# Performance work log

Measured on AMD Instinct MI355X. Metric: run time of the kernel, lower is better.

The kernel has to match this reference:

```python
import jax, jax.numpy as jnp
import numpy as np

N, E, G = 50000, 1600000, 512
H, NF_IN, NF_OUT, GF_OUT, EDIM, DEPTH = 128, 64, 64, 128, 16, 3
EPS = 1e-5


def seg_softmax(logits, seg, num):
    m = jax.ops.segment_max(logits, seg, num_segments=num)
    e = jnp.exp(logits - m[seg])
    s = jax.ops.segment_sum(e, seg, num_segments=num)
    return e / s[seg]


def batchnorm_train(x, gamma, beta):
    mu = jnp.mean(x, axis=0)
    var = jnp.mean((x - mu) ** 2, axis=0)  # biased, as torch BN training
    return (x - mu) * jax.lax.rsqrt(var + EPS) * gamma + beta


def setup_inputs() -> dict:
    key = jax.random.key(0)
    ks = jax.random.split(key, 20)
    inp = {}
    inp['x'] = jax.random.normal(ks[0], (N, NF_IN), jnp.float32)
    inp['edge_index'] = jax.random.randint(ks[1], (2, E), 0, N, jnp.int64)
    inp['edge_attr'] = jax.random.normal(ks[2], (E, EDIM), jnp.float32)
    inp['batch'] = jnp.sort(jax.random.randint(ks[3], (N,), 0, G, jnp.int64))
    inp['num_graphs'] = G
    s = 0.05
    inp['Wi'] = jax.random.normal(ks[4], (H, NF_IN), jnp.float32) * s
    inp['bi'] = jnp.zeros((H,), jnp.float32)
    inp['gat_W'] = jax.random.normal(ks[5], (DEPTH, H, 2 * H), jnp.float32) * s
    inp['gat_a'] = jax.random.normal(ks[6], (DEPTH, 2 * H), jnp.float32) * s
    inp['nfW1'] = jax.random.normal(ks[7], (H, H), jnp.float32) * s
    inp['nfb1'] = jnp.zeros((H,), jnp.float32)
    inp['nf_g'] = jnp.ones((H,), jnp.float32)
    inp['nf_b'] = jnp.zeros((H,), jnp.float32)
    inp['nfW2'] = jax.random.normal(ks[8], (NF_OUT, H), jnp.float32) * s
    inp['nfb2'] = jnp.zeros((NF_OUT,), jnp.float32)
    inp['gfW1'] = jax.random.normal(ks[9], (H, H), jnp.float32) * s
    inp['gfb1'] = jnp.zeros((H,), jnp.float32)
    inp['gf_g'] = jnp.ones((H,), jnp.float32)
    inp['gf_b'] = jnp.zeros((H,), jnp.float32)
    inp['gfW2'] = jax.random.normal(ks[10], (GF_OUT, H), jnp.float32) * s
    inp['gfb2'] = jnp.zeros((GF_OUT,), jnp.float32)
    return inp


def reference(x, edge_index, edge_attr, batch, num_graphs, Wi, bi, gat_W, gat_a,
              nfW1, nfb1, nf_g, nf_b, nfW2, nfb2,
              gfW1, gfb1, gf_g, gf_b, gfW2, gfb2):
    src, dst = edge_index[0], edge_index[1]
    nf = x @ Wi.T + bi  # [N,H]
    for i in range(DEPTH):
        src_nf = nf[src]            # [E,H]
        dst_nf = nf[dst]            # [E,H]
        ef = jnp.concatenate([src_nf, dst_nf], axis=-1) @ gat_a[i]  # [E]
        alpha = seg_softmax(ef, dst, N)
        agg = jax.ops.segment_sum(alpha[:, None] * src_nf, dst, num_segments=N)
        nf = jax.nn.relu(jnp.concatenate([nf, agg], axis=-1) @ gat_W[i].T)
    # 3-iteration attention pooling over graphs
    h = nf
    for _ in range(3):
        logits = jnp.sum(h * nf, axis=-1)  # [N]
        alpha = seg_softmax(logits, batch, num_graphs)
        h = alpha[:, None] * nf
    gf = jax.ops.segment_sum(h, batch, num_segments=num_graphs)  # [G,H]
    nf_out = jax.nn.relu(batchnorm_train(nf @ nfW1.T + nfb1, nf_g, nf_b)) @ nfW2.T + nfb2
    gf_out = jax.nn.relu(batchnorm_train(gf @ gfW1.T + gfb1, gf_g, gf_b)) @ gfW2.T + gfb2
    return nf_out, edge_attr, gf_out
```

## Files before the change

### kernel.cpp

```cpp
#include <hip/hip_runtime.h>

#define NN 50000
#define NE 1600000
#define NG 512
#define HD 128
#define NGRP 8
#define GRPSZ ((NN + NGRP - 1) / NGRP)
#define PCAP 28672

typedef __attribute__((ext_vector_type(8))) short bf16x8;
typedef __attribute__((ext_vector_type(4))) float f32x4;

static __device__ __forceinline__ unsigned bf16rn(float x) {
  unsigned b = __float_as_uint(x);
  return (b + 0x7FFFu + ((b >> 16) & 1u)) >> 16;
}
static __device__ __forceinline__ float bf16tof(unsigned short u) {
  return __uint_as_float(((unsigned)u) << 16);
}

__global__ void __launch_bounds__(256) k_part(const int* __restrict__ src,
                                              const int* __restrict__ dst,
                                              uint2* __restrict__ pairs,
                                              int* __restrict__ pcnt) {
  __shared__ uint2 buf[8][512];
  __shared__ int lcnt[8];
  __shared__ int gbase[8];
  __shared__ int nfl[8];
  const int tid = threadIdx.x;
  const int b = blockIdx.x & 7;
  if (tid < 8) lcnt[tid] = 0;
  __syncthreads();
  const int stride = gridDim.x * 256;
  for (int base_e = blockIdx.x * 256; base_e < NE; base_e += stride) {
    int e = base_e + tid;
    bool valid = e < NE;
    if (valid) {
      int d = dst[e];
      int s = src[e];
      int g = d / GRPSZ;
      int pos = atomicAdd(&lcnt[g], 1);
      buf[g][pos] = make_uint2((unsigned)d, (unsigned)s);
    }
    __syncthreads();
    if (tid < 8) {
      int c = lcnt[tid];
      int nf = (c >= 256) ? 256 : 0;
      nfl[tid] = nf;
      gbase[tid] = nf ? atomicAdd(&pcnt[tid * 8 + b], nf) : 0;
    }
    __syncthreads();
#pragma unroll
    for (int g0 = 0; g0 < 8; ++g0) {
      if (nfl[g0]) {
        int gb = gbase[g0] + tid;
        if (gb < PCAP)
          pairs[(size_t)(g0 * 8 + b) * PCAP + gb] = buf[g0][tid];
      }
    }
    __syncthreads();
#pragma unroll
    for (int g0 = 0; g0 < 8; ++g0) {
      if (nfl[g0]) {
        int rem = lcnt[g0] - 256;
        if (tid < rem) buf[g0][tid] = buf[g0][256 + tid];
      }
    }
    __syncthreads();
    if (tid < 8 && nfl[tid]) lcnt[tid] -= 256;
    __syncthreads();
  }
  if (tid < 8) {
    int c = lcnt[tid];
    gbase[tid] = c ? atomicAdd(&pcnt[tid * 8 + b], c) : 0;
  }
  __syncthreads();
#pragma unroll
  for (int g0 = 0; g0 < 8; ++g0) {
    int c = lcnt[g0];
    if (tid < c) {
      int gb = gbase[g0] + tid;
      if (gb < PCAP)
        pairs[(size_t)(g0 * 8 + b) * PCAP + gb] = buf[g0][tid];
    }
  }
}

__global__ void __launch_bounds__(256) k_hist(const uint2* __restrict__ pairs,
                                              const int* __restrict__ pcnt,
                                              int* __restrict__ hcnt) {
  __shared__ int hist[GRPSZ];
  const int b = blockIdx.x;
  const int g = b & 7, sub = b >> 3;
  const int li = g * 8 + sub;
  const int lo = g * GRPSZ;
  for (int i = threadIdx.x; i < GRPSZ; i += 256) hist[i] = 0;
  __syncthreads();
  int cnt = min(pcnt[li], PCAP);
  const uint2* lst = pairs + (size_t)li * PCAP;
  for (int i = threadIdx.x; i < cnt; i += 256)
    atomicAdd(&hist[(int)lst[i].x - lo], 1);
  __syncthreads();
  for (int i = threadIdx.x; i < GRPSZ; i += 256)
    hcnt[(size_t)li * GRPSZ + i] = hist[i];
}

__global__ void __launch_bounds__(256) k_csr(const uint2* __restrict__ pairs,
                                             const int* __restrict__ pcnt,
                                             const int* __restrict__ hcnt,
                                             int* __restrict__ row_ptr,
                                             int* __restrict__ csr_src) {
  __shared__ int rp[GRPSZ];
  __shared__ int cur[GRPSZ];
  __shared__ int wsum[256];
  const int b = blockIdx.x;
  const int g = b & 7, sub = b >> 3;
  const int li = g * 8 + sub;
  const int lo = g * GRPSZ;
  int gbase = 0;
  for (int gg = 0; gg < g; ++gg)
#pragma unroll
    for (int ss = 0; ss < 8; ++ss) gbase += pcnt[gg * 8 + ss];
  for (int i = threadIdx.x; i < GRPSZ; i += 256) {
    int dsum = 0, before = 0;
#pragma unroll
    for (int ss = 0; ss < 8; ++ss) {
      int h = hcnt[(size_t)(g * 8 + ss) * GRPSZ + i];
      dsum += h;
      if (ss < sub) before += h;
    }
    rp[i] = dsum;
    cur[i] = before;
  }
  __syncthreads();
  const int CH = (GRPSZ + 255) / 256;
  int t0 = threadIdx.x * CH;
  int t1 = min(GRPSZ, t0 + CH);
  int s = 0;
  for (int i = t0; i < t1; ++i) { int v = rp[i]; rp[i] = s; s += v; }
  wsum[threadIdx.x] = s;
  __syncthreads();
  for (int off = 1; off < 256; off <<= 1) {
    int t = ((int)threadIdx.x >= off) ? wsum[threadIdx.x - off] : 0;
    __syncthreads();
    wsum[threadIdx.x] += t;
    __syncthreads();
  }
  int add = gbase + ((threadIdx.x > 0) ? wsum[threadIdx.x - 1] : 0);
  for (int i = t0; i < t1; ++i) rp[i] += add;
  __syncthreads();
  for (int i = threadIdx.x; i < GRPSZ; i += 256) {
    cur[i] += rp[i];
    if (sub == 0) row_ptr[lo + i] = rp[i];
  }
  if (sub == 0 && g == 7 && threadIdx.x == 0) row_ptr[NN] = NE;
  __syncthreads();
  int cnt = min(pcnt[li], PCAP);
  const uint2* lst = pairs + (size_t)li * PCAP;
  for (int i = threadIdx.x; i < cnt; i += 256) {
    uint2 p = lst[i];
    int pos = atomicAdd(&cur[(int)p.x - lo], 1);
    csr_src[pos] = (int)p.y;
  }
}

__global__ void k_init_bounds(int* __restrict__ gs, int* __restrict__ ge) {
  int g = blockIdx.x * 256 + threadIdx.x;
  if (g < NG) { gs[g] = NN; ge[g] = 0; }
}
__global__ void k_bounds(const int* __restrict__ batch, int* __restrict__ gs, int* __restrict__ ge) {
  int n = blockIdx.x * 256 + threadIdx.x;
  if (n < NN) {
    int b = batch[n];
    atomicMin(&gs[b], n);
    atomicMax(&ge[b], n + 1);
  }
}

__global__ void k_cvt3(const float* __restrict__ a0, int n0,
                       const float* __restrict__ a1, int n1,
                       const float* __restrict__ a2, int n2,
                       unsigned short* __restrict__ b) {
  int i = blockIdx.x * 256 + threadIdx.x;
  if (i >= n0 + n1 + n2) return;
  float v = (i < n0) ? a0[i] : (i < n0 + n1) ? a1[i - n0] : a2[i - n0 - n1];
  b[i] = (unsigned short)bf16rn(v);
}

template <bool LAST>
__global__ void __launch_bounds__(512) k_layer(
    const unsigned short* __restrict__ nf16, const uint4* __restrict__ nf16u4,
    const float* __restrict__ e1in,
    const int* __restrict__ row_ptr, const int* __restrict__ csr_src,
    const unsigned short* __restrict__ W16, const float* __restrict__ dvec,
    unsigned short* __restrict__ out16, float* __restrict__ dout) {
  __shared__ unsigned short aggl[64][136];
  __shared__ float pdot[64];
  const int tid = threadIdx.x;
  const int wid = tid >> 6;
  const int lane = tid & 63;
  const int row0 = blockIdx.x * 64;
  if (tid < 64) pdot[tid] = 0.f;

  {
    const int q = lane >> 3;
    const int c = lane & 7;
    for (int r = 0; r < 8; ++r) {
      const int slot = wid * 8 + r;
      const int node = row0 + slot;
      int s = 0, e = 0;
      if (node < NN) { s = row_ptr[node]; e = row_ptr[node + 1]; }
      float acc[16];
#pragma unroll
      for (int i = 0; i < 16; ++i) acc[i] = 0.f;
      float zloc = 0.f;
      int j0 = s + q;      bool p0 = j0 < e;  int sc0 = p0 ? csr_src[j0] : 0;
      int j1 = s + 8 + q;  bool p1 = j1 < e;  int sc1 = p1 ? csr_src[j1] : 0;
      float w0 = p0 ? e1in[sc0] : 0.f;
      uint4 a0 = nf16u4[(size_t)sc0 * 16 + c * 2];
      uint4 a1 = nf16u4[(size_t)sc0 * 16 + c * 2 + 1];
      for (int j = s; j < e; j += 8) {
        int j2 = j + 16 + q; bool p2 = j2 < e;
        int sc2 = p2 ? csr_src[j2] : 0;
        float w1 = p1 ? e1in[sc1] : 0.f;
        uint4 b0 = nf16u4[(size_t)sc1 * 16 + c * 2];
        uint4 b1 = nf16u4[(size_t)sc1 * 16 + c * 2 + 1];
        zloc += w0;
        acc[0]  = fmaf(w0, __uint_as_float(a0.x << 16), acc[0]);
        acc[1]  = fmaf(w0, __uint_as_float(a0.x & 0xFFFF0000u), acc[1]);
        acc[2]  = fmaf(w0, __uint_as_float(a0.y << 16), acc[2]);
        acc[3]  = fmaf(w0, __uint_as_float(a0.y & 0xFFFF0000u), acc[3]);
        acc[4]  = fmaf(w0, __uint_as_float(a0.z << 16), acc[4]);
        acc[5]  = fmaf(w0, __uint_as_float(a0.z & 0xFFFF0000u), acc[5]);
        acc[6]  = fmaf(w0, __uint_as_float(a0.w << 16), acc[6]);
        acc[7]  = fmaf(w0, __uint_as_float(a0.w & 0xFFFF0000u), acc[7]);
        acc[8]  = fmaf(w0, __uint_as_float(a1.x << 16), acc[8]);
        acc[9]  = fmaf(w0, __uint_as_float(a1.x & 0xFFFF0000u), acc[9]);
        acc[10] = fmaf(w0, __uint_as_float(a1.y << 16), acc[10]);
        acc[11] = fmaf(w0, __uint_as_float(a1.y & 0xFFFF0000u), acc[11]);
        acc[12] = fmaf(w0, __uint_as_float(a1.z << 16), acc[12]);
        acc[13] = fmaf(w0, __uint_as_float(a1.z & 0xFFFF0000u), acc[13]);
        acc[14] = fmaf(w0, __uint_as_float(a1.w << 16), acc[14]);
        acc[15] = fmaf(w0, __uint_as_float(a1.w & 0xFFFF0000u), acc[15]);
        w0 = w1; a0 = b0; a1 = b1;
        sc1 = sc2; p1 = p2;
      }
      zloc += __shfl_xor(zloc, 8);
      zloc += __shfl_xor(zloc, 16);
      zloc += __shfl_xor(zloc, 32);
      float inv = (zloc > 0.f) ? 1.f / zloc : 0.f;
#pragma unroll
      for (int i = 0; i < 16; ++i) {
        acc[i] += __shfl_xor(acc[i], 8);
        acc[i] += __shfl_xor(acc[i], 16);
        acc[i] += __shfl_xor(acc[i], 32);
        acc[i] *= inv;
      }
      if (q == 0) {
        uint4 p0k, p1k;
        p0k.x = bf16rn(acc[0])  | (bf16rn(acc[1])  << 16);
        p0k.y = bf16rn(acc[2])  | (bf16rn(acc[3])  << 16);
        p0k.z = bf16rn(acc[4])  | (bf16rn(acc[5])  << 16);
        p0k.w = bf16rn(acc[6])  | (bf16rn(acc[7])  << 16);
        p1k.x = bf16rn(acc[8])  | (bf16rn(acc[9])  << 16);
        p1k.y = bf16rn(acc[10]) | (bf16rn(acc[11]) << 16);
        p1k.z = bf16rn(acc[12]) | (bf16rn(acc[13]) << 16);
        p1k.w = bf16rn(acc[14]) | (bf16rn(acc[15]) << 16);
        uint4* dst = (uint4*)(&aggl[slot][c * 16]);
        dst[0] = p0k;
        dst[1] = p1k;
      }
    }
  }
  __syncthreads();

  {
    const int lr = lane & 15;
    const int qq = lane >> 4;
    const int rblk = wid & 3, cblk = wid >> 2;
    const int rbase = row0 + rblk * 16;
    const int arow = min(rbase + lr, NN - 1);
    const unsigned short* pa1 = nf16 + (size_t)arow * 128;
    const unsigned short* pw = W16 + (size_t)(cblk * 64) * 256;

    f32x4 acc[4];
#pragma unroll
    for (int t = 0; t < 4; ++t) acc[t] = (f32x4){0.f, 0.f, 0.f, 0.f};

#pragma unroll
    for (int s = 0; s < 8; ++s) {
      bf16x8 af;
      if (s < 4) af = *(const bf16x8*)(pa1 + s * 32 + qq * 8);
      else       af = *(const bf16x8*)(&aggl[rblk * 16 + lr][(s - 4) * 32 + qq * 8]);
#pragma unroll
      for (int t = 0; t < 4; ++t) {
        bf16x8 bfr = *(const bf16x8*)(pw + (size_t)(t * 16 + lr) * 256 + s * 32 + qq * 8);
        acc[t] = __builtin_amdgcn_mfma_f32_16x16x32_bf16(af, bfr, acc[t], 0, 0, 0);
      }
    }

    float dv[4];
    if (!LAST) {
#pragma unroll
      for (int t = 0; t < 4; ++t) dv[t] = dvec[cblk * 64 + t * 16 + lr];
    }
    float p[4] = {0.f, 0.f, 0.f, 0.f};
#pragma unroll
    for (int j = 0; j < 4; ++j) {
      int n = rbase + qq * 4 + j;
      bool ok = n < NN;
#pragma unroll
      for (int t = 0; t < 4; ++t) {
        float v = fmaxf(acc[t][j], 0.f);
        if (ok) out16[(size_t)n * HD + cblk * 64 + t * 16 + lr] = (unsigned short)bf16rn(v);
        p[j] = fmaf(v, LAST ? v : dv[t], p[j]);
      }
      p[j] += __shfl_xor(p[j], 1);
      p[j] += __shfl_xor(p[j], 2);
      p[j] += __shfl_xor(p[j], 4);
      p[j] += __shfl_xor(p[j], 8);
    }
    if (lr == 0) {
#pragma unroll
      for (int j = 0; j < 4; ++j) atomicAdd(&pdot[rblk * 16 + qq * 4 + j], p[j]);
    }
  }
  __syncthreads();
  if (tid < 64) {
    int n = row0 + tid;
    if (n < NN) dout[n] = LAST ? pdot[tid] : __expf(pdot[tid]);
  }
}

__global__ void __launch_bounds__(256) k_head1(
    const unsigned short* __restrict__ A1, const unsigned short* __restrict__ W16,
    const float* __restrict__ bias, float* __restrict__ outf,
    float* __restrict__ statS, float* __restrict__ statQ) {
  __shared__ float bs[128], bq[128];
  const int l = threadIdx.x & 63;
  const int w = threadIdx.x >> 6;
  const int lr = l & 15;
  const int q = l >> 4;
  const int row0 = blockIdx.x * 64 + w * 16;
  const int arow = min(row0 + lr, NN - 1);
  const unsigned short* pa1 = A1 + (size_t)arow * 128;
  if (threadIdx.x < 128) { bs[threadIdx.x] = 0.f; bq[threadIdx.x] = 0.f; }

  f32x4 acc[8];
#pragma unroll
  for (int t = 0; t < 8; ++t) acc[t] = (f32x4){0.f, 0.f, 0.f, 0.f};
#pragma unroll
  for (int s = 0; s < 4; ++s) {
    bf16x8 af = *(const bf16x8*)(pa1 + s * 32 + q * 8);
#pragma unroll
    for (int t = 0; t < 8; ++t) {
      bf16x8 bfr = *(const bf16x8*)(W16 + (size_t)(t * 16 + lr) * 128 + s * 32 + q * 8);
      acc[t] = __builtin_amdgcn_mfma_f32_16x16x32_bf16(af, bfr, acc[t], 0, 0, 0);
    }
  }
  float bv[8];
#pragma unroll
  for (int t = 0; t < 8; ++t) bv[t] = bias[t * 16 + lr];
  float ps[8], pq[8];
#pragma unroll
  for (int t = 0; t < 8; ++t) { ps[t] = 0.f; pq[t] = 0.f; }
#pragma unroll
  for (int j = 0; j < 4; ++j) {
    int n = row0 + q * 4 + j;
    bool ok = n < NN;
#pragma unroll
    for (int t = 0; t < 8; ++t) {
      float v = acc[t][j] + bv[t];
      if (ok) {
        outf[(size_t)n * HD + t * 16 + lr] = v;
        ps[t] += v;
        pq[t] += v * v;
      }
    }
  }
  __syncthreads();
#pragma unroll
  for (int t = 0; t < 8; ++t) {
    ps[t] += __shfl_xor(ps[t], 16);
    ps[t] += __shfl_xor(ps[t], 32);
    pq[t] += __shfl_xor(pq[t], 16);
    pq[t] += __shfl_xor(pq[t], 32);
  }
  if (q == 0) {
#pragma unroll
    for (int t = 0; t < 8; ++t) {
      atomicAdd(&bs[t * 16 + lr], ps[t]);
      atomicAdd(&bq[t * 16 + lr], pq[t]);
    }
  }
  __syncthreads();
  if (threadIdx.x < 128) {
    atomicAdd(&statS[threadIdx.x], bs[threadIdx.x]);
    atomicAdd(&statQ[threadIdx.x], bq[threadIdx.x]);
  }
}

__global__ void __launch_bounds__(256) k_head2(
    const float* __restrict__ y, const unsigned short* __restrict__ W16,
    const float* __restrict__ bnA, const float* __restrict__ bnB,
    const float* __restrict__ bias, float* __restrict__ outf) {
  const int l = threadIdx.x & 63;
  const int w = threadIdx.x >> 6;
  const int lr = l & 15;
  const int q = l >> 4;
  const int row0 = blockIdx.x * 64 + w * 16;
  const int arow = min(row0 + lr, NN - 1);
  const float* py = y + (size_t)arow * 128;

  f32x4 acc[4];
#pragma unroll
  for (int t = 0; t < 4; ++t) acc[t] = (f32x4){0.f, 0.f, 0.f, 0.f};
#pragma unroll
  for (int s = 0; s < 4; ++s) {
    const int kg = s * 32 + q * 8;
    float4 y0 = *(const float4*)(py + kg);
    float4 y1 = *(const float4*)(py + kg + 4);
    float4 A0 = *(const float4*)(bnA + kg);
    float4 A1v = *(const float4*)(bnA + kg + 4);
    float4 B0 = *(const float4*)(bnB + kg);
    float4 B1v = *(const float4*)(bnB + kg + 4);
    bf16x8 af;
    af[0] = (short)bf16rn(fmaxf(fmaf(y0.x, A0.x, B0.x), 0.f));
    af[1] = (short)bf16rn(fmaxf(fmaf(y0.y, A0.y, B0.y), 0.f));
    af[2] = (short)bf16rn(fmaxf(fmaf(y0.z, A0.z, B0.z), 0.f));
    af[3] = (short)bf16rn(fmaxf(fmaf(y0.w, A0.w, B0.w), 0.f));
    af[4] = (short)bf16rn(fmaxf(fmaf(y1.x, A1v.x, B1v.x), 0.f));
    af[5] = (short)bf16rn(fmaxf(fmaf(y1.y, A1v.y, B1v.y), 0.f));
    af[6] = (short)bf16rn(fmaxf(fmaf(y1.z, A1v.z, B1v.z), 0.f));
    af[7] = (short)bf16rn(fmaxf(fmaf(y1.w, A1v.w, B1v.w), 0.f));
#pragma unroll
    for (int t = 0; t < 4; ++t) {
      bf16x8 bfr = *(const bf16x8*)(W16 + (size_t)(t * 16 + lr) * 128 + kg);
      acc[t] = __builtin_amdgcn_mfma_f32_16x16x32_bf16(af, bfr, acc[t], 0, 0, 0);
    }
  }
  float bv[4];
#pragma unroll
  for (int t = 0; t < 4; ++t) bv[t] = bias[t * 16 + lr];
#pragma unroll
  for (int j = 0; j < 4; ++j) {
    int n = row0 + q * 4 + j;
    if (n < NN) {
#pragma unroll
      for (int t = 0; t < 4; ++t)
        outf[(size_t)n * 64 + t * 16 + lr] = acc[t][j] + bv[t];
    }
  }
}

template <int K, int KA, int HO, bool PRE, bool RELUOUT, bool BIAS, bool OUT16, int DOTM>
__global__ void __launch_bounds__(256) k_gemm(
    const float* __restrict__ inA, const float* __restrict__ inB,
    const float* __restrict__ W, const float* __restrict__ bias,
    const float* __restrict__ preA, const float* __restrict__ preB,
    float* __restrict__ out, int nrows,
    unsigned* __restrict__ out16, const float* __restrict__ dvec,
    float* __restrict__ dout) {
  constexpr int KC = 64;
  constexpr int BM = 64;
  constexpr int MT = 4;
  constexpr int NT = HO / 16;
  constexpr int LDW = HO + 4;
  constexpr int LDA = KC + 4;

  __shared__ float Wl[KC * LDW];
  __shared__ float inl[BM * LDA];

  const int tid = threadIdx.x;
  const int tr = tid >> 4;
  const int tc = tid & 15;
  const int row0 = blockIdx.x * BM;
  const int r0 = tr * MT;
  const int c0 = tc * NT;

  float acc[MT][NT];
#pragma unroll
  for (int i = 0; i < MT; ++i)
#pragma unroll
    for (int j = 0; j < NT; ++j) acc[i][j] = BIAS ? bias[c0 + j] : 0.f;

  for (int cc = 0; cc < K / KC; ++cc) {
    const int k0 = cc * KC;
    if (cc) __syncthreads();
    for (int idx = tid; idx < HO * (KC / 4); idx += 256) {
      int h = idx >> 4;
      int qq = idx & 15;
      float4 w = *(const float4*)(W + (size_t)h * K + k0 + qq * 4);
      Wl[(qq * 4 + 0) * LDW + h] = w.x;
      Wl[(qq * 4 + 1) * LDW + h] = w.y;
      Wl[(qq * 4 + 2) * LDW + h] = w.z;
      Wl[(qq * 4 + 3) * LDW + h] = w.w;
    }
    for (int idx = tid; idx < BM * (KC / 4); idx += 256) {
      int r = idx >> 4;
      int qq = idx & 15;
      int n = row0 + r;
      int kg = k0 + qq * 4;
      float4 v = make_float4(0.f, 0.f, 0.f, 0.f);
      if (n < nrows) {
        if constexpr (KA == K) {
          v = *(const float4*)(inA + (size_t)n * K + kg);
        } else {
          if (k0 < KA) v = *(const float4*)(inA + (size_t)n * KA + kg);
          else         v = *(const float4*)(inB + (size_t)n * (K - KA) + kg - KA);
        }
      }
      if constexpr (PRE) {
        v.x = fmaxf(v.x * preA[kg + 0] + preB[kg + 0], 0.f);
        v.y = fmaxf(v.y * preA[kg + 1] + preB[kg + 1], 0.f);
        v.z = fmaxf(v.z * preA[kg + 2] + preB[kg + 2], 0.f);
        v.w = fmaxf(v.w * preA[kg + 3] + preB[kg + 3], 0.f);
      }
      *(float4*)(inl + r * LDA + qq * 4) = v;
    }
    __syncthreads();
#pragma unroll 8
    for (int k = 0; k < KC; ++k) {
      float a[MT];
#pragma unroll
      for (int i = 0; i < MT; ++i) a[i] = inl[(r0 + i) * LDA + k];
      float4 b0 = *(const float4*)(Wl + k * LDW + c0);
#pragma unroll
      for (int i = 0; i < MT; ++i) {
        acc[i][0] = fmaf(a[i], b0.x, acc[i][0]);
        acc[i][1] = fmaf(a[i], b0.y, acc[i][1]);
        acc[i][2] = fmaf(a[i], b0.z, acc[i][2]);
        acc[i][3] = fmaf(a[i], b0.w, acc[i][3]);
      }
      if constexpr (NT == 8) {
        float4 b1 = *(const float4*)(Wl + k * LDW + c0 + 4);
#pragma unroll
        for (int i = 0; i < MT; ++i) {
          acc[i][4] = fmaf(a[i], b1.x, acc[i][4]);
          acc[i][5] = fmaf(a[i], b1.y, acc[i][5]);
          acc[i][6] = fmaf(a[i], b1.z, acc[i][6]);
          acc[i][7] = fmaf(a[i], b1.w, acc[i][7]);
        }
      }
    }
  }
  float dv[DOTM == 1 ? NT : 1];
  if constexpr (DOTM == 1) {
#pragma unroll
    for (int j = 0; j < NT; ++j) dv[j] = dvec[c0 + j];
  }
#pragma unroll
  for (int i = 0; i < MT; ++i) {
    int n = row0 + r0 + i;
    if constexpr (RELUOUT) {
#pragma unroll
      for (int j = 0; j < NT; ++j) acc[i][j] = fmaxf(acc[i][j], 0.f);
    }
    if (n < nrows) {
      float4 o0 = make_float4(acc[i][0], acc[i][1], acc[i][2], acc[i][3]);
      *(float4*)(out + (size_t)n * HO + c0) = o0;
      if constexpr (NT == 8) {
        float4 o1 = make_float4(acc[i][4], acc[i][5], acc[i][6], acc[i][7]);
        *(float4*)(out + (size_t)n * HO + c0 + 4) = o1;
      }
      if constexpr (OUT16 && NT == 8) {
        uint4 pk;
        pk.x = bf16rn(acc[i][0]) | (bf16rn(acc[i][1]) << 16);
        pk.y = bf16rn(acc[i][2]) | (bf16rn(acc[i][3]) << 16);
        pk.z = bf16rn(acc[i][4]) | (bf16rn(acc[i][5]) << 16);
        pk.w = bf16rn(acc[i][6]) | (bf16rn(acc[i][7]) << 16);
        *(uint4*)(out16 + (size_t)n * 64 + tc * 4) = pk;
      }
    }
    if constexpr (DOTM != 0) {
      float p = 0.f;
#pragma unroll
      for (int j = 0; j < NT; ++j)
        p = fmaf(acc[i][j], (DOTM == 1) ? dv[j] : acc[i][j], p);
      p += __shfl_xor(p, 1);
      p += __shfl_xor(p, 2);
      p += __shfl_xor(p, 4);
      p += __shfl_xor(p, 8);
      if (tc == 0 && n < nrows) dout[n] = (DOTM == 1) ? __expf(p) : p;
    }
  }
}

__global__ void k_pool(const unsigned short* __restrict__ nf16, const float* __restrict__ r,
                       const int* __restrict__ gs, const int* __restrict__ ge,
                       float* __restrict__ alpha, float* __restrict__ gf) {
  int g = blockIdx.x;
  int s = gs[g], e = ge[g];
  __shared__ float red[256];
  for (int it = 0; it < 3; ++it) {
    float lm = -INFINITY;
    for (int n = s + threadIdx.x; n < e; n += 256) {
      float l = r[n];
      if (it) l *= alpha[n];
      lm = fmaxf(lm, l);
    }
    red[threadIdx.x] = lm;
    __syncthreads();
    for (int off = 128; off > 0; off >>= 1) {
      if ((int)threadIdx.x < off) red[threadIdx.x] = fmaxf(red[threadIdx.x], red[threadIdx.x + off]);
      __syncthreads();
    }
    float m = red[0];
    __syncthreads();
    float zz = 0.f;
    for (int n = s + threadIdx.x; n < e; n += 256) {
      float l = r[n];
      if (it) l *= alpha[n];
      zz += __expf(l - m);
    }
    red[threadIdx.x] = zz;
    __syncthreads();
    for (int off = 128; off > 0; off >>= 1) {
      if ((int)threadIdx.x < off) red[threadIdx.x] += red[threadIdx.x + off];
      __syncthreads();
    }
    float z = red[0];
    __syncthreads();
    float invz = 1.f / z;
    for (int n = s + threadIdx.x; n < e; n += 256) {
      float l = r[n];
      if (it) l *= alpha[n];
      alpha[n] = __expf(l - m) * invz;
    }
    __syncthreads();
  }
  int c = threadIdx.x & 127;
  int rr2 = threadIdx.x >> 7;
  float acc = 0.f;
  for (int n = s + rr2; n < e; n += 2)
    acc += alpha[n] * bf16tof(nf16[(size_t)n * HD + c]);
  red[threadIdx.x] = acc;
  __syncthreads();
  if (rr2 == 0) gf[(size_t)g * HD + c] = red[threadIdx.x] + red[threadIdx.x + 128];
}

__global__ void k_colstats(const float* __restrict__ y, float* __restrict__ sum,
                           float* __restrict__ sumsq, int R, int CH) {
  int c = threadIdx.x & 127;
  int rr = threadIdx.x >> 7;
  int r0 = blockIdx.x * CH;
  int r1 = min(R, r0 + CH);
  float s = 0.f, q = 0.f;
  for (int r = r0 + rr; r < r1; r += 2) {
    float v = y[(size_t)r * HD + c];
    s += v;
    q += v * v;
  }
  __shared__ float ls[256], lq[256];
  ls[threadIdx.x] = s;
  lq[threadIdx.x] = q;
  __syncthreads();
  if (rr == 0) {
    s += ls[threadIdx.x + 128];
    q += lq[threadIdx.x + 128];
    atomicAdd(&sum[c], s);
    atomicAdd(&sumsq[c], q);
  }
}

__global__ void k_bn_final(const float* __restrict__ sum, const float* __restrict__ sumsq,
                           const float* __restrict__ g, const float* __restrict__ b,
                           float* __restrict__ A, float* __restrict__ B, float R) {
  int c = threadIdx.x;
  float mu = sum[c] / R;
  float var = sumsq[c] / R - mu * mu;
  float a = g[c] * rsqrtf(var + 1e-5f);
  A[c] = a;
  B[c] = b[c] - mu * a;
}

__global__ void k_copy4(const float4* __restrict__ a, float4* __restrict__ b, int n) {
  int i = blockIdx.x * 256 + threadIdx.x;
  if (i < n) b[i] = a[i];
}

extern "C" void kernel_launch(void* const* d_in, const int* in_sizes, int n_in,
                              void* d_out, int out_size, void* d_ws, size_t ws_size,
                              hipStream_t stream) {
  const float* x        = (const float*)d_in[0];
  const int*   ei       = (const int*)d_in[1];
  const float* edge_attr= (const float*)d_in[2];
  const int*   batch    = (const int*)d_in[3];
  const float* Wi       = (const float*)d_in[5];
  const float* bi       = (const float*)d_in[6];
  const float* gat_W    = (const float*)d_in[7];
  const float* gat_a    = (const float*)d_in[8];
  const float* nfW1     = (const float*)d_in[9];
  const float* nfb1     = (const float*)d_in[10];
  const float* nf_g     = (const float*)d_in[11];
  const float* nf_b     = (const float*)d_in[12];
  const float* nfW2     = (const float*)d_in[13];
  const float* nfb2     = (const float*)d_in[14];
  const float* gfW1     = (const float*)d_in[15];
  const float* gfb1     = (const float*)d_in[16];
  const float* gf_g     = (const float*)d_in[17];
  const float* gf_b     = (const float*)d_in[18];
  const float* gfW2     = (const float*)d_in[19];
  const float* gfb2     = (const float*)d_in[20];

  float* out = (float*)d_out;

  unsigned short* nf16A = (unsigned short*)d_ws;
  unsigned short* nf16B = nf16A + (size_t)NN * HD;
  unsigned short* wt_gat = nf16B + (size_t)NN * HD;
  unsigned short* wt_nf1 = wt_gat + 3 * 128 * 256;
  unsigned short* wt_nf2 = wt_nf1 + 128 * 128;
  float* nfA   = (float*)(wt_nf2 + 64 * 128);
  float* e1A   = nfA + (size_t)NN * HD;
  float* e1B   = e1A + NN;
  float* rv    = e1B + NN;
  float* alpha = rv + NN;
  float* gf    = alpha + NN;
  float* gy    = gf + (size_t)NG * HD;
  int*   pcnt  = (int*)(gy + (size_t)NG * HD);
  float* sums  = (float*)(pcnt + 64);
  float* sums2 = sums + 256;
  float* bnAB  = sums2 + 256;
  int* row_ptr = (int*)(bnAB + 256);
  int* csr_src = row_ptr + NN + 1;
  int* gs      = csr_src + NE;
  int* ge      = gs + NG;
  int* hcnt    = ge + NG;
  uint2* pairs = (uint2*)nfA;

  const int* src  = ei;
  const int* dstp = ei + NE;

  hipMemsetAsync(pcnt, 0, (64 + 512) * sizeof(int), stream);

  k_part<<<512, 256, 0, stream>>>(src, dstp, pairs, pcnt);
  k_hist<<<64, 256, 0, stream>>>(pairs, pcnt, hcnt);
  k_csr<<<64, 256, 0, stream>>>(pairs, pcnt, hcnt, row_ptr, csr_src);

  k_init_bounds<<<2, 256, 0, stream>>>(gs, ge);
  k_bounds<<<(NN + 255) / 256, 256, 0, stream>>>(batch, gs, ge);

  k_cvt3<<<(3 * 128 * 256 + 128 * 128 + 64 * 128 + 255) / 256, 256, 0, stream>>>(
      gat_W, 3 * 128 * 256, nfW1, 128 * 128, nfW2, 64 * 128, wt_gat);

  k_gemm<64, 64, 128, false, false, true, true, 1><<<(NN + 63) / 64, 256, 0, stream>>>(
      x, nullptr, Wi, bi, nullptr, nullptr, nfA, NN, (unsigned*)nf16A, gat_a, e1A);

  const int layer_grid = (NN + 63) / 64;
  k_layer<false><<<layer_grid, 512, 0, stream>>>(
      nf16A, (const uint4*)nf16A, e1A, row_ptr, csr_src,
      wt_gat + 0 * 128 * 256, gat_a + 1 * 256, nf16B, e1B);
  k_layer<false><<<layer_grid, 512, 0, stream>>>(
      nf16B, (const uint4*)nf16B, e1B, row_ptr, csr_src,
      wt_gat + 1 * 128 * 256, gat_a + 2 * 256, nf16A, e1A);
  k_layer<true><<<layer_grid, 512, 0, stream>>>(
      nf16A, (const uint4*)nf16A, e1A, row_ptr, csr_src,
      wt_gat + 2 * 128 * 256, nullptr, nf16B, rv);
  unsigned short* cur = nf16B;

  k_pool<<<NG, 256, 0, stream>>>(cur, rv, gs, ge, alpha, gf);

  const int gemm_grid = (NN + 63) / 64;
  k_head1<<<gemm_grid, 256, 0, stream>>>(cur, wt_nf1, nfb1, nfA, sums, sums + 128);
  k_bn_final<<<1, 128, 0, stream>>>(sums, sums + 128, nf_g, nf_b, bnAB, bnAB + 128, (float)NN);
  k_head2<<<gemm_grid, 256, 0, stream>>>(nfA, wt_nf2, bnAB, bnAB + 128, nfb2, out);

  k_gemm<128, 128, 128, false, false, true, false, 0><<<(NG + 63) / 64, 256, 0, stream>>>(
      gf, nullptr, gfW1, gfb1, nullptr, nullptr, gy, NG, nullptr, nullptr, nullptr);
  k_colstats<<<4, 256, 0, stream>>>(gy, sums2, sums2 + 128, NG, 128);
  k_bn_final<<<1, 128, 0, stream>>>(sums2, sums2 + 128, gf_g, gf_b, bnAB, bnAB + 128, (float)NG);
  k_gemm<128, 128, 128, true, false, true, false, 0><<<(NG + 63) / 64, 256, 0, stream>>>(
      gy, nullptr, gfW2, gfb2, bnAB, bnAB + 128,
      out + (size_t)NN * 64 + (size_t)NE * 16, NG, nullptr, nullptr, nullptr);

  int n4 = NE * 16 / 4;
  k_copy4<<<(n4 + 255) / 256, 256, 0, stream>>>((const float4*)edge_attr,
                                                (float4*)(out + (size_t)NN * 64), n4);
}
```

Before: 613.0 us.

## Quantize gathered node features to int8 with per-row scales for neighbor aggregation

The neighbor-aggregation gather now reads int8 node features (offset by 128) with a per-node scale stored next to the softmax numerator in a float2, halving the bytes gathered per edge compared with bf16. The producing GEMM and layer epilogues compute a per-row max (via shared-memory atomicMax) and write the quantized copy alongside the bf16 copy. The first GEMM also stops writing the unused fp32 output. This trades accuracy in the aggregated features and adds extra epilogue work, writes and a block barrier in exchange for less random-gather memory traffic.

New measurement: 610.0 us. Within noise of the previous version (-0.5%).

```diff
diff --git a/kernel.cpp b/kernel.cpp
--- a/kernel.cpp
+++ b/kernel.cpp
@@ -189,18 +189,21 @@
 
 template <bool LAST>
 __global__ void __launch_bounds__(512) k_layer(
-    const unsigned short* __restrict__ nf16, const uint4* __restrict__ nf16u4,
-    const float* __restrict__ e1in,
+    const unsigned short* __restrict__ nf16, const uint4* __restrict__ nf8u4,
+    const float2* __restrict__ es_in,
     const int* __restrict__ row_ptr, const int* __restrict__ csr_src,
     const unsigned short* __restrict__ W16, const float* __restrict__ dvec,
-    unsigned short* __restrict__ out16, float* __restrict__ dout) {
+    unsigned short* __restrict__ out16,
+    unsigned char* __restrict__ nf8out, float2* __restrict__ es_out,
+    float* __restrict__ dout) {
   __shared__ unsigned short aggl[64][136];
   __shared__ float pdot[64];
+  __shared__ int rmaxI[64];
   const int tid = threadIdx.x;
   const int wid = tid >> 6;
   const int lane = tid & 63;
   const int row0 = blockIdx.x * 64;
-  if (tid < 64) pdot[tid] = 0.f;
+  if (tid < 64) { pdot[tid] = 0.f; rmaxI[tid] = 0; }
 
   {
     const int q = lane >> 3;
@@ -213,48 +216,53 @@
       float acc[16];
 #pragma unroll
       for (int i = 0; i < 16; ++i) acc[i] = 0.f;
-      float zloc = 0.f;
+      float zloc = 0.f, wsl = 0.f;
       int j0 = s + q;      bool p0 = j0 < e;  int sc0 = p0 ? csr_src[j0] : 0;
       int j1 = s + 8 + q;  bool p1 = j1 < e;  int sc1 = p1 ? csr_src[j1] : 0;
-      float w0 = p0 ? e1in[sc0] : 0.f;
-      uint4 a0 = nf16u4[(size_t)sc0 * 16 + c * 2];
-      uint4 a1 = nf16u4[(size_t)sc0 * 16 + c * 2 + 1];
+      float2 e0 = es_in[sc0];
+      float w0  = p0 ? e0.x : 0.f;
+      float ws0 = p0 ? e0.x * e0.y : 0.f;
+      uint4 a = nf8u4[(size_t)sc0 * 8 + c];
       for (int j = s; j < e; j += 8) {
         int j2 = j + 16 + q; bool p2 = j2 < e;
         int sc2 = p2 ? csr_src[j2] : 0;
-        float w1 = p1 ? e1in[sc1] : 0.f;
-        uint4 b0 = nf16u4[(size_t)sc1 * 16 + c * 2];
-        uint4 b1 = nf16u4[(size_t)sc1 * 16 + c * 2 + 1];
-        zloc += w0;
-        acc[0]  = fmaf(w0, __uint_as_float(a0.x << 16), acc[0]);
-        acc[1]  = fmaf(w0, __uint_as_float(a0.x & 0xFFFF0000u), acc[1]);
-        acc[2]  = fmaf(w0, __uint_as_float(a0.y << 16), acc[2]);
-        acc[3]  = fmaf(w0, __uint_as_float(a0.y & 0xFFFF0000u), acc[3]);
-        acc[4]  = fmaf(w0, __uint_as_float(a0.z << 16), acc[4]);
-        acc[5]  = fmaf(w0, __uint_as_float(a0.z & 0xFFFF0000u), acc[5]);
-        acc[6]  = fmaf(w0, __uint_as_float(a0.w << 16), acc[6]);
-        acc[7]  = fmaf(w0, __uint_as_float(a0.w & 0xFFFF0000u), acc[7]);
-        acc[8]  = fmaf(w0, __uint_as_float(a1.x << 16), acc[8]);
-        acc[9]  = fmaf(w0, __uint_as_float(a1.x & 0xFFFF0000u), acc[9]);
-        acc[10] = fmaf(w0, __uint_as_float(a1.y << 16), acc[10]);
-        acc[11] = fmaf(w0, __uint_as_float(a1.y & 0xFFFF0000u), acc[11]);
-        acc[12] = fmaf(w0, __uint_as_float(a1.z << 16), acc[12]);
-        acc[13] = fmaf(w0, __uint_as_float(a1.z & 0xFFFF0000u), acc[13]);
-        acc[14] = fmaf(w0, __uint_as_float(a1.w << 16), acc[14]);
-        acc[15] = fmaf(w0, __uint_as_float(a1.w & 0xFFFF0000u), acc[15]);
-        w0 = w1; a0 = b0; a1 = b1;
-        sc1 = sc2; p1 = p2;
+        float2 e1v = es_in[sc1];
+        uint4 b = nf8u4[(size_t)sc1 * 8 + c];
+        float w1  = p1 ? e1v.x : 0.f;
+        float ws1 = p1 ? e1v.x * e1v.y : 0.f;
+        zloc += w0; wsl += ws0;
+        acc[0]  = fmaf(ws0, (float)(a.x & 255u), acc[0]);
+        acc[1]  = fmaf(ws0, (float)((a.x >> 8) & 255u), acc[1]);
+        acc[2]  = fmaf(ws0, (float)((a.x >> 16) & 255u), acc[2]);
+        acc[3]  = fmaf(ws0, (float)(a.x >> 24), acc[3]);
+        acc[4]  = fmaf(ws0, (float)(a.y & 255u), acc[4]);
+        acc[5]  = fmaf(ws0, (float)((a.y >> 8) & 255u), acc[5]);
+        acc[6]  = fmaf(ws0, (float)((a.y >> 16) & 255u), acc[6]);
+        acc[7]  = fmaf(ws0, (float)(a.y >> 24), acc[7]);
+        acc[8]  = fmaf(ws0, (float)(a.z & 255u), acc[8]);
+        acc[9]  = fmaf(ws0, (float)((a.z >> 8) & 255u), acc[9]);
+        acc[10] = fmaf(ws0, (float)((a.z >> 16) & 255u), acc[10]);
+        acc[11] = fmaf(ws0, (float)(a.z >> 24), acc[11]);
+        acc[12] = fmaf(ws0, (float)(a.w & 255u), acc[12]);
+        acc[13] = fmaf(ws0, (float)((a.w >> 8) & 255u), acc[13]);
+        acc[14] = fmaf(ws0, (float)((a.w >> 16) & 255u), acc[14]);
+        acc[15] = fmaf(ws0, (float)(a.w >> 24), acc[15]);
+        w0 = w1; ws0 = ws1; a = b; sc1 = sc2; p1 = p2;
       }
       zloc += __shfl_xor(zloc, 8);
       zloc += __shfl_xor(zloc, 16);
       zloc += __shfl_xor(zloc, 32);
+      wsl += __shfl_xor(wsl, 8);
+      wsl += __shfl_xor(wsl, 16);
+      wsl += __shfl_xor(wsl, 32);
       float inv = (zloc > 0.f) ? 1.f / zloc : 0.f;
+      float base = 128.f * wsl;
 #pragma unroll
       for (int i = 0; i < 16; ++i) {
         acc[i] += __shfl_xor(acc[i], 8);
         acc[i] += __shfl_xor(acc[i], 16);
         acc[i] += __shfl_xor(acc[i], 32);
-        acc[i] *= inv;
+        acc[i] = (acc[i] - base) * inv;
       }
       if (q == 0) {
         uint4 p0k, p1k;
@@ -309,10 +317,14 @@
     for (int j = 0; j < 4; ++j) {
       int n = rbase + qq * 4 + j;
       bool ok = n < NN;
+      int slot = n - row0;
 #pragma unroll
       for (int t = 0; t < 4; ++t) {
         float v = fmaxf(acc[t][j], 0.f);
-        if (ok) out16[(size_t)n * HD + cblk * 64 + t * 16 + lr] = (unsigned short)bf16rn(v);
+        if (ok) {
+          out16[(size_t)n * HD + cblk * 64 + t * 16 + lr] = (unsigned short)bf16rn(v);
+          if (!LAST) atomicMax(&rmaxI[slot], __float_as_int(v));
+        }
         p[j] = fmaf(v, LAST ? v : dv[t], p[j]);
       }
       p[j] += __shfl_xor(p[j], 1);
@@ -324,11 +336,32 @@
 #pragma unroll
       for (int j = 0; j < 4; ++j) atomicAdd(&pdot[rblk * 16 + qq * 4 + j], p[j]);
     }
-  }
-  __syncthreads();
+    __syncthreads();
+    if (!LAST) {
+#pragma unroll
+      for (int j = 0; j < 4; ++j) {
+        int n = rbase + qq * 4 + j;
+        if (n < NN) {
+          int slot = n - row0;
+          float m = __int_as_float(rmaxI[slot]);
+          float is = (m > 0.f) ? 127.f / m : 0.f;
+#pragma unroll
+          for (int t = 0; t < 4; ++t) {
+            float v = fmaxf(acc[t][j], 0.f);
+            int u = __float2int_rn(v * is) + 128;
+            nf8out[(size_t)n * HD + cblk * 64 + t * 16 + lr] = (unsigned char)u;
+          }
+        }
+      }
+    }
+  }
   if (tid < 64) {
     int n = row0 + tid;
-    if (n < NN) dout[n] = LAST ? pdot[tid] : __expf(pdot[tid]);
+    if (n < NN) {
+      if (LAST) dout[n] = pdot[tid];
+      else      es_out[n] = make_float2(__expf(pdot[tid]),
+                                        __int_as_float(rmaxI[tid]) * (1.f / 127.f));
+    }
   }
 }
 
@@ -453,14 +486,16 @@
   }
 }
 
-template <int K, int KA, int HO, bool PRE, bool RELUOUT, bool BIAS, bool OUT16, int DOTM>
+template <int K, int KA, int HO, bool PRE, bool RELUOUT, bool BIAS, bool OUT16,
+          bool OUTF32, int DOTM, bool Q8>
 __global__ void __launch_bounds__(256) k_gemm(
     const float* __restrict__ inA, const float* __restrict__ inB,
     const float* __restrict__ W, const float* __restrict__ bias,
     const float* __restrict__ preA, const float* __restrict__ preB,
     float* __restrict__ out, int nrows,
     unsigned* __restrict__ out16, const float* __restrict__ dvec,
-    float* __restrict__ dout) {
+    float* __restrict__ dout,
+    unsigned char* __restrict__ nf8, float2* __restrict__ es) {
   constexpr int KC = 64;
   constexpr int BM = 64;
   constexpr int MT = 4;
@@ -557,11 +592,13 @@
       for (int j = 0; j < NT; ++j) acc[i][j] = fmaxf(acc[i][j], 0.f);
     }
     if (n < nrows) {
-      float4 o0 = make_float4(acc[i][0], acc[i][1], acc[i][2], acc[i][3]);
-      *(float4*)(out + (size_t)n * HO + c0) = o0;
-      if constexpr (NT == 8) {
-        float4 o1 = make_float4(acc[i][4], acc[i][5], acc[i][6], acc[i][7]);
-        *(float4*)(out + (size_t)n * HO + c0 + 4) = o1;
+      if constexpr (OUTF32) {
+        float4 o0 = make_float4(acc[i][0], acc[i][1], acc[i][2], acc[i][3]);
+        *(float4*)(out + (size_t)n * HO + c0) = o0;
+        if constexpr (NT == 8) {
+          float4 o1 = make_float4(acc[i][4], acc[i][5], acc[i][6], acc[i][7]);
+          *(float4*)(out + (size_t)n * HO + c0 + 4) = o1;
+        }
       }
       if constexpr (OUT16 && NT == 8) {
         uint4 pk;
@@ -572,6 +609,29 @@
         *(uint4*)(out16 + (size_t)n * 64 + tc * 4) = pk;
       }
     }
+    float s_row = 0.f;
+    if constexpr (Q8 && NT == 8) {
+      float mx = 0.f;
+#pragma unroll
+      for (int j = 0; j < NT; ++j) mx = fmaxf(mx, fabsf(acc[i][j]));
+      mx = fmaxf(mx, __shfl_xor(mx, 1));
+      mx = fmaxf(mx, __shfl_xor(mx, 2));
+      mx = fmaxf(mx, __shfl_xor(mx, 4));
+      mx = fmaxf(mx, __shfl_xor(mx, 8));
+      s_row = mx * (1.f / 127.f);
+      float is = (mx > 0.f) ? 127.f / mx : 0.f;
+      if (n < nrows) {
+        unsigned b0 = 0, b1 = 0;
+#pragma unroll
+        for (int j = 0; j < 4; ++j)
+          b0 |= (unsigned)(__float2int_rn(acc[i][j] * is) + 128) << (8 * j);
+#pragma unroll
+        for (int j = 4; j < 8; ++j)
+          b1 |= (unsigned)(__float2int_rn(acc[i][j] * is) + 128) << (8 * (j - 4));
+        uint2 pk8 = make_uint2(b0, b1);
+        *(uint2*)(nf8 + (size_t)n * HO + c0) = pk8;
+      }
+    }
     if constexpr (DOTM != 0) {
       float p = 0.f;
 #pragma unroll
@@ -581,7 +641,10 @@
       p += __shfl_xor(p, 2);
       p += __shfl_xor(p, 4);
       p += __shfl_xor(p, 8);
-      if (tc == 0 && n < nrows) dout[n] = (DOTM == 1) ? __expf(p) : p;
+      if (tc == 0 && n < nrows) {
+        if constexpr (Q8) es[n] = make_float2(__expf(p), s_row);
+        else dout[n] = (DOTM == 1) ? __expf(p) : p;
+      }
     }
   }
 }
@@ -705,27 +768,30 @@
 
   float* out = (float*)d_out;
 
-  unsigned short* nf16A = (unsigned short*)d_ws;
-  unsigned short* nf16B = nf16A + (size_t)NN * HD;
-  unsigned short* wt_gat = nf16B + (size_t)NN * HD;
-  unsigned short* wt_nf1 = wt_gat + 3 * 128 * 256;
-  unsigned short* wt_nf2 = wt_nf1 + 128 * 128;
-  float* nfA   = (float*)(wt_nf2 + 64 * 128);
-  float* e1A   = nfA + (size_t)NN * HD;
-  float* e1B   = e1A + NN;
-  float* rv    = e1B + NN;
-  float* alpha = rv + NN;
-  float* gf    = alpha + NN;
-  float* gy    = gf + (size_t)NG * HD;
-  int*   pcnt  = (int*)(gy + (size_t)NG * HD);
-  float* sums  = (float*)(pcnt + 64);
-  float* sums2 = sums + 256;
-  float* bnAB  = sums2 + 256;
-  int* row_ptr = (int*)(bnAB + 256);
-  int* csr_src = row_ptr + NN + 1;
-  int* gs      = csr_src + NE;
-  int* ge      = gs + NG;
-  int* hcnt    = ge + NG;
+  char* wp = (char*)d_ws;
+  unsigned short* nf16A = (unsigned short*)wp; wp += (size_t)NN * HD * 2;
+  unsigned short* nf16B = (unsigned short*)wp; wp += (size_t)NN * HD * 2;
+  unsigned short* wt_gat = (unsigned short*)wp; wp += (size_t)3 * 128 * 256 * 2;
+  unsigned short* wt_nf1 = (unsigned short*)wp; wp += 128 * 128 * 2;
+  unsigned short* wt_nf2 = (unsigned short*)wp; wp += 64 * 128 * 2;
+  unsigned char* nf8A = (unsigned char*)wp; wp += (size_t)NN * HD;
+  unsigned char* nf8B = (unsigned char*)wp; wp += (size_t)NN * HD;
+  float* nfA = (float*)wp; wp += (size_t)NN * HD * 4;
+  float2* esA = (float2*)wp; wp += (size_t)NN * 8;
+  float2* esB = (float2*)wp; wp += (size_t)NN * 8;
+  float* rv = (float*)wp; wp += (size_t)NN * 4;
+  float* alpha = (float*)wp; wp += (size_t)NN * 4;
+  float* gf = (float*)wp; wp += (size_t)NG * HD * 4;
+  float* gy = (float*)wp; wp += (size_t)NG * HD * 4;
+  int* pcnt = (int*)wp; wp += 64 * 4;
+  float* sums = (float*)wp; wp += 256 * 4;
+  float* sums2 = (float*)wp; wp += 256 * 4;
+  float* bnAB = (float*)wp; wp += 256 * 4;
+  int* row_ptr = (int*)wp; wp += (size_t)(NN + 1) * 4;
+  int* csr_src = (int*)wp; wp += (size_t)NE * 4;
+  int* gs = (int*)wp; wp += NG * 4;
+  int* ge = (int*)wp; wp += NG * 4;
+  int* hcnt = (int*)wp; wp += (size_t)64 * GRPSZ * 4;
   uint2* pairs = (uint2*)nfA;
 
   const int* src  = ei;
@@ -743,19 +809,21 @@
   k_cvt3<<<(3 * 128 * 256 + 128 * 128 + 64 * 128 + 255) / 256, 256, 0, stream>>>(
       gat_W, 3 * 128 * 256, nfW1, 128 * 128, nfW2, 64 * 128, wt_gat);
 
-  k_gemm<64, 64, 128, false, false, true, true, 1><<<(NN + 63) / 64, 256, 0, stream>>>(
-      x, nullptr, Wi, bi, nullptr, nullptr, nfA, NN, (unsigned*)nf16A, gat_a, e1A);
+  k_gemm<64, 64, 128, false, false, true, true, false, 1, true>
+      <<<(NN + 63) / 64, 256, 0, stream>>>(
+      x, nullptr, Wi, bi, nullptr, nullptr, nullptr, NN,
+      (unsigned*)nf16A, gat_a, nullptr, nf8A, esA);
 
   const int layer_grid = (NN + 63) / 64;
   k_layer<false><<<layer_grid, 512, 0, stream>>>(
-      nf16A, (const uint4*)nf16A, e1A, row_ptr, csr_src,
-      wt_gat + 0 * 128 * 256, gat_a + 1 * 256, nf16B, e1B);
+      nf16A, (const uint4*)nf8A, esA, row_ptr, csr_src,
+      wt_gat + 0 * 128 * 256, gat_a + 1 * 256, nf16B, nf8B, esB, nullptr);
   k_layer<false><<<layer_grid, 512, 0, stream>>>(
-      nf16B, (const uint4*)nf16B, e1B, row_ptr, csr_src,
-      wt_gat + 1 * 128 * 256, gat_a + 2 * 256, nf16A, e1A);
+      nf16B, (const uint4*)nf8B, esB, row_ptr, csr_src,
+      wt_gat + 1 * 128 * 256, gat_a + 2 * 256, nf16A, nf8A, esA, nullptr);
   k_layer<true><<<layer_grid, 512, 0, stream>>>(
-      nf16A, (const uint4*)nf16A, e1A, row_ptr, csr_src,
-      wt_gat + 2 * 128 * 256, nullptr, nf16B, rv);
+      nf16A, (const uint4*)nf8A, esA, row_ptr, csr_src,
+      wt_gat + 2 * 128 * 256, nullptr, nf16B, nullptr, nullptr, rv);
   unsigned short* cur = nf16B;
 
   k_pool<<<NG, 256, 0, stream>>>(cur, rv, gs, ge, alpha, gf);
@@ -765,13 +833,17 @@
   k_bn_final<<<1, 128, 0, stream>>>(sums, sums + 128, nf_g, nf_b, bnAB, bnAB + 128, (float)NN);
   k_head2<<<gemm_grid, 256, 0, stream>>>(nfA, wt_nf2, bnAB, bnAB + 128, nfb2, out);
 
-  k_gemm<128, 128, 128, false, false, true, false, 0><<<(NG + 63) / 64, 256, 0, stream>>>(
-      gf, nullptr, gfW1, gfb1, nullptr, nullptr, gy, NG, nullptr, nullptr, nullptr);
+  k_gemm<128, 128, 128, false, false, true, false, true, 0, false>
+      <<<(NG + 63) / 64, 256, 0, stream>>>(
+      gf, nullptr, gfW1, gfb1, nullptr, nullptr, gy, NG,
+      nullptr, nullptr, nullptr, nullptr, nullptr);
   k_colstats<<<4, 256, 0, stream>>>(gy, sums2, sums2 + 128, NG, 128);
   k_bn_final<<<1, 128, 0, stream>>>(sums2, sums2 + 128, gf_g, gf_b, bnAB, bnAB + 128, (float)NG);
-  k_gemm<128, 128, 128, true, false, true, false, 0><<<(NG + 63) / 64, 256, 0, stream>>>(
+  k_gemm<128, 128, 128, true, false, true, false, true, 0, false>
+      <<<(NG + 63) / 64, 256, 0, stream>>>(
       gy, nullptr, gfW2, gfb2, bnAB, bnAB + 128,
-      out + (size_t)NN * 64 + (size_t)NE * 16, NG, nullptr, nullptr, nullptr);
+      out + (size_t)NN * 64 + (size_t)NE * 16, NG,
+      nullptr, nullptr, nullptr, nullptr, nullptr);
 
   int n4 = NE * 16 / 4;
   k_copy4<<<(n4 + 255) / 256, 256, 0, stream>>>((const float4*)edge_attr,
```
